# Kernel optimization log

Hardware: AMD Instinct MI355X
Metric: run time of the kernel (lower is better)

## Reference

```python
import jax, jax.numpy as jnp
import numpy as np

EMBED_DIM = 2048
NUM_HEADS = 16
HEAD_DIM = EMBED_DIM // NUM_HEADS


def setup_inputs() -> dict:
    key = jax.random.key(0)
    k_x, k_qkv, k_out = jax.random.split(key, 3)
    x = jax.random.normal(k_x, (4, 2048, EMBED_DIM), dtype=jnp.float32)
    # torch nn.Linear(in, out) weight is [out, in]; y = x @ W.T
    scale = 1.0 / np.sqrt(EMBED_DIM)
    W_qkv = jax.random.uniform(k_qkv, (3 * EMBED_DIM, EMBED_DIM), dtype=jnp.float32, minval=-scale, maxval=scale)
    W_out = jax.random.uniform(k_out, (EMBED_DIM, EMBED_DIM), dtype=jnp.float32, minval=-scale, maxval=scale)
    return {"x": x, "W_qkv": W_qkv, "W_out": W_out}


def reference(x, W_qkv, W_out):
    B, T, C = x.shape
    H, D = NUM_HEADS, HEAD_DIM
    qkv = jnp.einsum("btc,fc->btf", x, W_qkv)  # [B,T,3C]
    q, k, v = jnp.split(qkv, 3, axis=-1)
    q = q.reshape(B, T, H, D).transpose(0, 2, 1, 3)  # [B,H,T,D]
    k = k.reshape(B, T, H, D).transpose(0, 2, 1, 3)
    v = v.reshape(B, T, H, D).transpose(0, 2, 1, 3)
    att = jnp.einsum("bhqd,bhkd->bhqk", q, k) / jnp.sqrt(jnp.float32(D))
    causal = jnp.tril(jnp.ones((T, T), dtype=bool))
    att = jnp.where(causal[None, None], att, -jnp.inf)
    att = jax.nn.softmax(att, axis=-1)
    out = jnp.einsum("bhqk,bhkd->bhqd", att, v)  # [B,H,T,D]
    out = out.transpose(0, 2, 1, 3).reshape(B, T, C)
    return jnp.einsum("btc,oc->bto", out, W_out)
```

## Files before the change

### kernel.cpp

```cpp
#include <hip/hip_runtime.h>
#include <hip/hip_bf16.h>
#include <math.h>

#define BDIM 4
#define TDIM 2048
#define CDIM 2048
#define HDIM 16
#define DDIM 128
#define MROWS (BDIM*TDIM)
#define NQKV (3*CDIM)
#define GK   CDIM
#define QSZ  (MROWS*CDIM)

#define NTILES 32
#define NITER  16
#define HT     8192
#define BOFF   32768

#define QSCALE 0.1275171f

typedef __attribute__((ext_vector_type(8))) short short8;
typedef __attribute__((ext_vector_type(4))) unsigned short ushort4v;
typedef __attribute__((ext_vector_type(4))) float f32x4;

__device__ __forceinline__ unsigned short f2bf(float f) {
    unsigned int u = __float_as_uint(f);
    u += 0x7fffu + ((u >> 16) & 1u);
    return (unsigned short)(u >> 16);
}

__device__ __forceinline__ void gload16(const unsigned short* g, unsigned short* l) {
    __builtin_amdgcn_global_load_lds((__attribute__((address_space(1))) void*)(g),
                                     (__attribute__((address_space(3))) void*)(l),
                                     16, 0, 0);
}

__global__ __launch_bounds__(256) void cvt_bf16(const float* __restrict__ in,
                                                unsigned short* __restrict__ outp,
                                                int n4, int sbound)
{
    const int stride = gridDim.x * blockDim.x;
    for (int i = blockIdx.x * blockDim.x + threadIdx.x; i < n4; i += stride) {
        float4 f = ((const float4*)in)[i];
        const float s = (i < sbound) ? QSCALE : 1.0f;
        ushort4v u;
        u[0] = f2bf(f.x*s); u[1] = f2bf(f.y*s); u[2] = f2bf(f.z*s); u[3] = f2bf(f.w*s);
        ((ushort4v*)outp)[i] = u;
    }
}

__device__ __forceinline__ void stage_half(const unsigned short* __restrict__ T,
                                           int rowbase, int kcol,
                                           unsigned short* dst, int w, int lane)
{
    const int sw = ((lane & 3) ^ ((lane >> 3) & 3)) * 8;
#pragma unroll
    for (int j = 0; j < 2; ++j) {
        const int r = w*32 + j*16 + (lane >> 2);
        gload16(T + (size_t)(rowbase + r)*GK + kcol + sw, dst + (w*32 + j*16)*32);
    }
}

template<int MQ, int KS, int BUF, bool RDB, bool WAIT>
__device__ __forceinline__ void gphase(unsigned short* lds,
    const unsigned short* __restrict__ stT, int stRow, int stKcol, unsigned short* stDst,
    int wr, int wc, int fr, int colu, int w, int lane,
    short8 (&bfr)[4], f32x4 (&acc)[8][4])
{
    const unsigned short* Ah = lds + (BUF*2 + KS)*HT;
    const unsigned short* Bh = lds + BOFF + (BUF*2 + KS)*HT;
    short8 af[4];
#pragma unroll
    for (int mi = 0; mi < 4; ++mi)
        af[mi] = *(const short8*)&Ah[(wr*128 + (MQ*4 + mi)*16 + fr)*32 + colu];
    if (RDB) {
#pragma unroll
        for (int nj = 0; nj < 4; ++nj)
            bfr[nj] = *(const short8*)&Bh[(wc*64 + nj*16 + fr)*32 + colu];
    }
    stage_half(stT, stRow, stKcol, stDst, w, lane);
    if (WAIT) asm volatile("s_waitcnt vmcnt(4)" ::: "memory");
    __builtin_amdgcn_s_barrier();
    asm volatile("s_waitcnt lgkmcnt(0)" ::: "memory");
    __builtin_amdgcn_sched_barrier(0);
    __builtin_amdgcn_s_setprio(1);
#pragma unroll
    for (int mi = 0; mi < 4; ++mi)
#pragma unroll
        for (int nj = 0; nj < 4; ++nj)
            acc[MQ*4 + mi][nj] = __builtin_amdgcn_mfma_f32_16x16x32_bf16(af[mi], bfr[nj], acc[MQ*4 + mi][nj], 0, 0, 0);
    __builtin_amdgcn_s_setprio(0);
    __builtin_amdgcn_s_barrier();
}

template<int MODE>
__global__ __launch_bounds__(512, 2) void gemm8(const unsigned short* __restrict__ A,
                                                const unsigned short* __restrict__ B,
                                                float* __restrict__ outp,
                                                unsigned short* __restrict__ qb,
                                                unsigned short* __restrict__ kb,
                                                unsigned short* __restrict__ vt,
                                                int Nsz)
{
    extern __shared__ unsigned short lds[];
    const int tid  = threadIdx.x;
    const int w    = tid >> 6;
    const int lane = tid & 63;
    const int wr   = w >> 2, wc = w & 3;
    const int fr   = lane & 15;
    const int fg   = lane >> 4;
    const int colu = (fg ^ ((fr >> 1) & 3)) * 8;
    const int m0   = blockIdx.x * 256, n0 = blockIdx.y * 256;

    f32x4 acc[8][4];
#pragma unroll
    for (int i = 0; i < 8; ++i)
#pragma unroll
        for (int j = 0; j < 4; ++j) acc[i][j] = (f32x4)(0.f);
    short8 bfr[4];

    stage_half(A, m0, 0,  lds,             w, lane);
    stage_half(B, n0, 0,  lds + BOFF,      w, lane);
    stage_half(A, m0, 32, lds + HT,        w, lane);
    stage_half(B, n0, 32, lds + BOFF + HT, w, lane);
    stage_half(A, m0, 64, lds + 2*HT,        w, lane);
    stage_half(B, n0, 64, lds + BOFF + 2*HT, w, lane);
    asm volatile("s_waitcnt vmcnt(0)" ::: "memory");
    __builtin_amdgcn_s_barrier();

    for (int i = 0; i < NITER; ++i) {
        const int t1 = 2*i + 1;
        const int t2 = (2*i + 2 < NTILES) ? 2*i + 2 : 0;
        const int t3 = (2*i + 3 < NTILES) ? 2*i + 3 : 0;
        gphase<0,0,0,true ,false>(lds, A, m0, t1*64+32, lds + 3*HT,        wr, wc, fr, colu, w, lane, bfr, acc);
        gphase<1,0,0,false,false>(lds, B, n0, t1*64+32, lds + BOFF + 3*HT, wr, wc, fr, colu, w, lane, bfr, acc);
        gphase<0,1,0,true ,false>(lds, A, m0, t2*64,    lds,               wr, wc, fr, colu, w, lane, bfr, acc);
        gphase<1,1,0,false,true >(lds, B, n0, t2*64,    lds + BOFF,        wr, wc, fr, colu, w, lane, bfr, acc);
        gphase<0,0,1,true ,false>(lds, A, m0, t2*64+32, lds + HT,          wr, wc, fr, colu, w, lane, bfr, acc);
        gphase<1,0,1,false,false>(lds, B, n0, t2*64+32, lds + BOFF + HT,   wr, wc, fr, colu, w, lane, bfr, acc);
        gphase<0,1,1,true ,false>(lds, A, m0, t3*64,    lds + 2*HT,        wr, wc, fr, colu, w, lane, bfr, acc);
        gphase<1,1,1,false,true >(lds, B, n0, t3*64,    lds + BOFF + 2*HT, wr, wc, fr, colu, w, lane, bfr, acc);
    }
    asm volatile("s_waitcnt vmcnt(0)" ::: "memory");

    if (MODE == 0) {
#pragma unroll
        for (int mi = 0; mi < 8; ++mi)
#pragma unroll
            for (int nj = 0; nj < 4; ++nj) {
                const int n   = n0 + wc*64 + nj*16 + fr;
                const int sel = n >> 11;
                const int c   = n & 2047;
                const int hh  = c >> 7, dd = c & 127;
                const int mb  = m0 + wr*128 + mi*16 + fg*4;
                const int bb  = mb >> 11, tt = mb & 2047;
                if (sel == 2) {
                    ushort4v v;
#pragma unroll
                    for (int r = 0; r < 4; ++r) v[r] = f2bf(acc[mi][nj][r]);
                    *(ushort4v*)&vt[((size_t)(bb*HDIM + hh)*DDIM + dd)*TDIM + tt] = v;
                } else {
                    unsigned short* dstb = (sel == 0) ? qb : kb;
#pragma unroll
                    for (int r = 0; r < 4; ++r)
                        dstb[((size_t)(bb*HDIM + hh)*TDIM + tt + r)*DDIM + dd] = f2bf(acc[mi][nj][r]);
                }
            }
    } else {
#pragma unroll
        for (int mi = 0; mi < 8; ++mi)
#pragma unroll
            for (int nj = 0; nj < 4; ++nj) {
                const int n = n0 + wc*64 + nj*16 + fr;
#pragma unroll
                for (int r = 0; r < 4; ++r) {
                    const int m = m0 + wr*128 + mi*16 + fg*4 + r;
                    outp[(size_t)m*Nsz + n] = acc[mi][nj][r];
                }
            }
    }
}

__global__ __launch_bounds__(512) void attn_mfma(const unsigned short* __restrict__ Qg,
                                                 const unsigned short* __restrict__ Kg,
                                                 const unsigned short* __restrict__ Vt,
                                                 unsigned short* __restrict__ attb)
{
    extern __shared__ unsigned short smem[];
    unsigned short* KsB = smem;
    unsigned short* VsB = smem + 16384;
    unsigned short* Ps  = smem + 32768;

    const int tid  = threadIdx.x;
    const int w    = tid >> 6;
    const int lane = tid & 63;
    const int g    = lane >> 4;
    const int c    = lane & 15;
    const int bh   = blockIdx.x & 63;
    const int qb_  = 15 - (blockIdx.x >> 6);
    const int q0   = qb_ * 128;
    const int qt   = 2*qb_ + 1;
    const int qw   = q0 + w*16;

    const unsigned short* Kbh  = Kg + (size_t)bh*TDIM*DDIM;
    const unsigned short* Vtbh = Vt + (size_t)bh*DDIM*TDIM;

    short8 qf[4];
    {
        const unsigned short* qrow = Qg + ((size_t)bh*TDIM + qw + c)*DDIM + g*8;
#pragma unroll
        for (int s = 0; s < 4; ++s)
            qf[s] = *(const short8*)(qrow + s*32);
    }

    short8 onesf;
#pragma unroll
    for (int j = 0; j < 8; ++j) onesf[j] = (short)0x3F80;

    f32x4 oacc[8];
#pragma unroll
    for (int i = 0; i < 8; ++i) oacc[i] = (f32x4)(0.f);
    float m_r[4], l_r[4];
#pragma unroll
    for (int r = 0; r < 4; ++r) { m_r[r] = -INFINITY; l_r[r] = 0.f; }

#define STAGE_K(buf, kt_)                                                        \
    {                                                                            \
        _Pragma("unroll")                                                        \
        for (int j = 0; j < 2; ++j) {                                            \
            const int rw  = (w<<3) + (j<<2) + (lane >> 4);                       \
            const int sub = (lane & 15) ^ (rw & 7);                              \
            gload16(Kbh + ((size_t)((kt_)*64 + rw))*DDIM + sub*8,                \
                    &KsB[(buf)*8192 + ((w<<3) + (j<<2))*128]);                   \
        }                                                                        \
    }
#define STAGE_V(buf, kt_)                                                        \
    {                                                                            \
        _Pragma("unroll")                                                        \
        for (int j = 0; j < 2; ++j) {                                            \
            const int d   = (w<<4) + (j<<3) + (lane >> 3);                       \
            const int sub = (lane & 7) ^ (d & 7);                                \
            gload16(Vtbh + (size_t)d*TDIM + (kt_)*64 + sub*8,                    \
                    &VsB[(buf)*8192 + ((w<<4) + (j<<3))*64]);                    \
        }                                                                        \
    }

    STAGE_K(0, 0);
    STAGE_V(0, 0);
    __syncthreads();

    for (int kt = 0; kt <= qt; ++kt) {
        const int cur = kt & 1;
        if (kt < qt) { STAGE_K(cur ^ 1, kt + 1); STAGE_V(cur ^ 1, kt + 1); }

        const bool active = (kt*64) <= (qw + 15);

        if (active) {
            f32x4 sa[4];
#pragma unroll
            for (int n = 0; n < 4; ++n) sa[n] = (f32x4)(0.f);
#pragma unroll
            for (int s = 0; s < 4; ++s)
#pragma unroll
                for (int n = 0; n < 4; ++n) {
                    const int row = n*16 + c;
                    short8 bf = *(const short8*)&KsB[cur*8192 + ((row*128 + s*32 + g*8) ^ ((row&7)<<3))];
                    sa[n] = __builtin_amdgcn_mfma_f32_16x16x32_bf16(qf[s], bf, sa[n], 0, 0, 0);
                }

            if (kt*64 + 63 > qw) {
#pragma unroll
                for (int n = 0; n < 4; ++n) {
                    const int kgl = kt*64 + n*16 + c;
#pragma unroll
                    for (int r = 0; r < 4; ++r) {
                        const int qgl = qw + g*4 + r;
                        if (kgl > qgl) sa[n][r] = -INFINITY;
                    }
                }
            }

            f32x4 p[4];
            bool slow = (kt == 0);
            if (!slow) {
#pragma unroll
                for (int n = 0; n < 4; ++n)
#pragma unroll
                    for (int r = 0; r < 4; ++r)
                        p[n][r] = exp2f(sa[n][r] - m_r[r]);
                float pm = p[0][0];
#pragma unroll
                for (int n = 0; n < 4; ++n)
#pragma unroll
                    for (int r = 0; r < 4; ++r)
                        pm = fmaxf(pm, p[n][r]);
                slow = __any(pm > 256.0f);
            }
            if (slow) {
                float corr[4];
#pragma unroll
                for (int r = 0; r < 4; ++r) {
                    float mx = fmaxf(fmaxf(sa[0][r], sa[1][r]), fmaxf(sa[2][r], sa[3][r]));
                    mx = fmaxf(mx, __shfl_xor(mx, 1));
                    mx = fmaxf(mx, __shfl_xor(mx, 2));
                    mx = fmaxf(mx, __shfl_xor(mx, 4));
                    mx = fmaxf(mx, __shfl_xor(mx, 8));
                    const float mn = fmaxf(m_r[r], mx);
                    corr[r] = exp2f(m_r[r] - mn);
                    m_r[r] = mn;
                }
#pragma unroll
                for (int n = 0; n < 4; ++n)
#pragma unroll
                    for (int r = 0; r < 4; ++r)
                        p[n][r] = exp2f(sa[n][r] - m_r[r]);
#pragma unroll
                for (int i = 0; i < 8; ++i) {
                    f32x4 o = oacc[i];
                    o[0] *= corr[0]; o[1] *= corr[1]; o[2] *= corr[2]; o[3] *= corr[3];
                    oacc[i] = o;
                }
#pragma unroll
                for (int r = 0; r < 4; ++r) l_r[r] *= corr[r];
            }

            unsigned short* Pw = &Ps[w*1024];
#pragma unroll
            for (int n = 0; n < 4; ++n)
#pragma unroll
                for (int r = 0; r < 4; ++r) {
                    const int q = g*4 + r, k = n*16 + c;
                    Pw[(q*64 + k) ^ ((q&7)<<3)] = f2bf(p[n][r]);
                }
            short8 pf[2];
#pragma unroll
            for (int s2 = 0; s2 < 2; ++s2)
                pf[s2] = *(const short8*)&Pw[(c*64 + s2*32 + g*8) ^ ((c&7)<<3)];

            f32x4 rs = (f32x4)(0.f);
            rs = __builtin_amdgcn_mfma_f32_16x16x32_bf16(pf[0], onesf, rs, 0, 0, 0);
            rs = __builtin_amdgcn_mfma_f32_16x16x32_bf16(pf[1], onesf, rs, 0, 0, 0);
#pragma unroll
            for (int r = 0; r < 4; ++r) l_r[r] += rs[r];

#pragma unroll
            for (int s2 = 0; s2 < 2; ++s2)
#pragma unroll
                for (int dt = 0; dt < 8; ++dt) {
                    const int d = dt*16 + c;
                    short8 vf = *(const short8*)&VsB[cur*8192 + ((d*64 + s2*32 + g*8) ^ ((d&7)<<3))];
                    oacc[dt] = __builtin_amdgcn_mfma_f32_16x16x32_bf16(pf[s2], vf, oacc[dt], 0, 0, 0);
                }
        }

        __syncthreads();
    }

    float inv[4];
#pragma unroll
    for (int r = 0; r < 4; ++r) inv[r] = 1.f / l_r[r];
    const int b = bh >> 4, h = bh & 15;
    unsigned short* obase = attb + ((size_t)b*TDIM + qw + g*4)*CDIM + h*DDIM + c;
#pragma unroll
    for (int dt = 0; dt < 8; ++dt)
#pragma unroll
        for (int r = 0; r < 4; ++r)
            obase[(size_t)r*CDIM + dt*16] = f2bf(oacc[dt][r] * inv[r]);
}

extern "C" void kernel_launch(void* const* d_in, const int* in_sizes, int n_in,
                              void* d_out, int out_size, void* d_ws, size_t ws_size,
                              hipStream_t stream)
{
    const float* x    = (const float*)d_in[0];
    const float* Wqkv = (const float*)d_in[1];
    const float* Wout = (const float*)d_in[2];
    float* out = (float*)d_out;

    unsigned short* ws = (unsigned short*)d_ws;
    unsigned short* xb    = ws;
    unsigned short* Wqkvb = xb    + (size_t)MROWS*CDIM;
    unsigned short* Woutb = Wqkvb + (size_t)NQKV*CDIM;
    unsigned short* Qb    = Woutb + (size_t)CDIM*CDIM;
    unsigned short* Kb    = Qb + QSZ;
    unsigned short* Vtb   = Kb + QSZ;
    unsigned short* attb  = Vtb + QSZ;

    cvt_bf16<<<2048, 256, 0, stream>>>(x,    xb,    MROWS*CDIM/4, 0);
    cvt_bf16<<<2048, 256, 0, stream>>>(Wqkv, Wqkvb, NQKV*CDIM/4, CDIM*CDIM/4);
    cvt_bf16<<<1024, 256, 0, stream>>>(Wout, Woutb, CDIM*CDIM/4, 0);
    gemm8<0><<<dim3(MROWS/256, NQKV/256), 512, 131072, stream>>>(xb, Wqkvb, nullptr, Qb, Kb, Vtb, NQKV);
    attn_mfma<<<dim3(64*16), 512, 81920, stream>>>(Qb, Kb, Vtb, attb);
    gemm8<1><<<dim3(MROWS/256, CDIM/256), 512, 131072, stream>>>(attb, Woutb, out, nullptr, nullptr, nullptr, CDIM);
}
```

Before: 417.0 us.

## Fuse bf16 conversion launches and remap GEMM tiles per XCD for L2 locality

The three fp32-to-bf16 conversion launches are merged into a single kernel that loops over x, W_qkv and W_out, removing two launches and their gaps. Both GEMMs now remap the linear block id so that each of the 8 XCDs (assigned round-robin by block id) works on a contiguous rectangular region of output tiles. This gives each XCD's private L2 more shared A and B panels. The remap assumes the grid dimensions divide evenly by RX and by 8, which holds for the fixed shapes here.

Result: no change. 419.2 us (+0.5%).

```diff
diff --git a/kernel.cpp b/kernel.cpp
--- a/kernel.cpp
+++ b/kernel.cpp
@@ -35,17 +35,33 @@
                                      16, 0, 0);
 }
 
-__global__ __launch_bounds__(256) void cvt_bf16(const float* __restrict__ in,
-                                                unsigned short* __restrict__ outp,
-                                                int n4, int sbound)
+__global__ __launch_bounds__(256) void cvt_all(const float* __restrict__ x,
+                                               const float* __restrict__ wqkv,
+                                               const float* __restrict__ wout,
+                                               unsigned short* __restrict__ xb,
+                                               unsigned short* __restrict__ wqkvb,
+                                               unsigned short* __restrict__ woutb)
 {
     const int stride = gridDim.x * blockDim.x;
-    for (int i = blockIdx.x * blockDim.x + threadIdx.x; i < n4; i += stride) {
-        float4 f = ((const float4*)in)[i];
-        const float s = (i < sbound) ? QSCALE : 1.0f;
+    const int t0 = blockIdx.x * blockDim.x + threadIdx.x;
+    for (int i = t0; i < MROWS*CDIM/4; i += stride) {
+        float4 f = ((const float4*)x)[i];
         ushort4v u;
-        u[0] = f2bf(f.x*s); u[1] = f2bf(f.y*s); u[2] = f2bf(f.z*s); u[3] = f2bf(f.w*s);
-        ((ushort4v*)outp)[i] = u;
+        u[0]=f2bf(f.x); u[1]=f2bf(f.y); u[2]=f2bf(f.z); u[3]=f2bf(f.w);
+        ((ushort4v*)xb)[i] = u;
+    }
+    for (int i = t0; i < NQKV*CDIM/4; i += stride) {
+        float4 f = ((const float4*)wqkv)[i];
+        const float s = (i < CDIM*CDIM/4) ? QSCALE : 1.0f;
+        ushort4v u;
+        u[0]=f2bf(f.x*s); u[1]=f2bf(f.y*s); u[2]=f2bf(f.z*s); u[3]=f2bf(f.w*s);
+        ((ushort4v*)wqkvb)[i] = u;
+    }
+    for (int i = t0; i < CDIM*CDIM/4; i += stride) {
+        float4 f = ((const float4*)wout)[i];
+        ushort4v u;
+        u[0]=f2bf(f.x); u[1]=f2bf(f.y); u[2]=f2bf(f.z); u[3]=f2bf(f.w);
+        ((ushort4v*)woutb)[i] = u;
     }
 }
 
@@ -93,7 +109,7 @@
     __builtin_amdgcn_s_barrier();
 }
 
-template<int MODE>
+template<int MODE, int RX>
 __global__ __launch_bounds__(512, 2) void gemm8(const unsigned short* __restrict__ A,
                                                 const unsigned short* __restrict__ B,
                                                 float* __restrict__ outp,
@@ -110,7 +126,16 @@
     const int fr   = lane & 15;
     const int fg   = lane >> 4;
     const int colu = (fg ^ ((fr >> 1) & 3)) * 8;
-    const int m0   = blockIdx.x * 256, n0 = blockIdx.y * 256;
+
+    const int gx  = gridDim.x, gy = gridDim.y;
+    const int id  = blockIdx.x + blockIdx.y * gx;
+    const int xcd = id & 7;
+    const int jj  = id >> 3;
+    const int mx  = gx / RX;
+    const int my  = (gy * RX) >> 3;
+    const int bx  = (xcd % RX) * mx + (jj % mx);
+    const int by  = (xcd / RX) * my + (jj / mx);
+    const int m0  = bx * 256, n0 = by * 256;
 
     f32x4 acc[8][4];
 #pragma unroll
@@ -386,10 +411,8 @@
     unsigned short* Vtb   = Kb + QSZ;
     unsigned short* attb  = Vtb + QSZ;
 
-    cvt_bf16<<<2048, 256, 0, stream>>>(x,    xb,    MROWS*CDIM/4, 0);
-    cvt_bf16<<<2048, 256, 0, stream>>>(Wqkv, Wqkvb, NQKV*CDIM/4, CDIM*CDIM/4);
-    cvt_bf16<<<1024, 256, 0, stream>>>(Wout, Woutb, CDIM*CDIM/4, 0);
-    gemm8<0><<<dim3(MROWS/256, NQKV/256), 512, 131072, stream>>>(xb, Wqkvb, nullptr, Qb, Kb, Vtb, NQKV);
+    cvt_all<<<2048, 256, 0, stream>>>(x, Wqkv, Wout, xb, Wqkvb, Woutb);
+    gemm8<0,4><<<dim3(MROWS/256, NQKV/256), 512, 131072, stream>>>(xb, Wqkvb, nullptr, Qb, Kb, Vtb, NQKV);
     attn_mfma<<<dim3(64*16), 512, 81920, stream>>>(Qb, Kb, Vtb, attb);
-    gemm8<1><<<dim3(MROWS/256, CDIM/256), 512, 131072, stream>>>(attb, Woutb, out, nullptr, nullptr, nullptr, CDIM);
-}
+    gemm8<1,2><<<dim3(MROWS/256, CDIM/256), 512, 131072, stream>>>(attb, Woutb, out, nullptr, nullptr, nullptr, CDIM);
+}
```
